# Kernel tuning notes

Measured on AMD Instinct MI355X. Metric: run time of the kernel, lower is better.

Reference implementation:

```python
import jax, jax.numpy as jnp
import numpy as np

N_NODES = 20000
N_EDGES = 400000
B = 4            # number of edge_attr tensors in the Python loop (batch of graphs)
NODE_DIM = 256   # == hidden_dim (required: forward feeds raw x into edge_fc)
EDGE_DIM = 16
HIDDEN = 256
OUT_DIM = 128


def setup_inputs() -> dict:
    key = jax.random.key(0)
    ks = jax.random.split(key, 6)
    x = jax.random.normal(ks[0], (N_NODES, NODE_DIM), dtype=jnp.float32)
    edge_index = jax.random.randint(ks[1], (2, N_EDGES), 0, N_NODES, dtype=jnp.int64)
    edge_attrs = jax.random.normal(ks[2], (B, N_EDGES, EDGE_DIM), dtype=jnp.float32)
    fan_in = 2 * HIDDEN + EDGE_DIM  # edge_fc in_features
    W_edge = jax.random.normal(ks[3], (fan_in, HIDDEN), dtype=jnp.float32) / np.sqrt(fan_in).astype(np.float32)
    b_edge = jnp.zeros((HIDDEN,), dtype=jnp.float32)
    W_graph = jax.random.normal(ks[4], (HIDDEN, OUT_DIM), dtype=jnp.float32) / np.sqrt(HIDDEN).astype(np.float32)
    b_graph = jnp.zeros((OUT_DIM,), dtype=jnp.float32)
    return {"x": x, "edge_index": edge_index, "edge_attrs": edge_attrs,
            "W_edge": W_edge, "b_edge": b_edge, "W_graph": W_graph, "b_graph": b_graph}


def reference(x, edge_index, edge_attrs, W_edge, b_edge, W_graph, b_graph):
    # Original: for each edge_attr in edge_attrs:
    #   relu(cat([x[src], x[dst], edge_attr]) @ W_edge + b).mean(0) @ W_graph + b_graph
    # Equivalent: split W_edge by the concat blocks; the (src,dst) contribution is
    # shared across the batch, so compute it once and broadcast.
    D = x.shape[1]
    W_src, W_dst, W_attr = W_edge[:D], W_edge[D:2 * D], W_edge[2 * D:]
    src = x[edge_index[0]]                      # [E, D] gather
    dst = x[edge_index[1]]                      # [E, D] gather
    base = src @ W_src + dst @ W_dst + b_edge   # [E, H]
    h = jax.nn.relu(base[None, :, :] + jnp.einsum('bea,ah->beh', edge_attrs, W_attr))  # [B, E, H]
    graph_feat = h.mean(axis=1)                 # [B, H] mean pool over edges
    return graph_feat @ W_graph + b_graph       # [B, OUT]
```

## Files before the change

kernel.cpp:

```cpp
#include <hip/hip_runtime.h>

#define N_NODES 20000
#define N_EDGES 400000
#define NODE_DIM 256
#define HIDDEN 256
#define OUT_DIM 128
#define PROJ_BLOCKS 628
#define CONV_BLOCKS 1024
#define EDGE_GRID 3125
#define NPART 8
#define ROWP 40

typedef __attribute__((ext_vector_type(8))) short short8;
typedef __attribute__((ext_vector_type(4))) float f32x4;

__device__ inline unsigned short f2bf(float f) {
  union { float f; unsigned u; } v; v.f = f;
  unsigned r = (v.u + 0x7FFFu + ((v.u >> 16) & 1u)) >> 16;
  return (unsigned short)r;
}

__global__ __launch_bounds__(256) void proj_mfma(
    const float* __restrict__ x, const float* __restrict__ We,
    const float* __restrict__ be, unsigned short* __restrict__ C,
    float* __restrict__ partial, const float* __restrict__ attrs,
    unsigned short* __restrict__ attrs_bf) {
  const int tid = threadIdx.x;
  if (blockIdx.x >= PROJ_BLOCKS) {
    const int nt = CONV_BLOCKS * 256;
    const int total4 = 4 * N_EDGES * 16 / 4;
    for (int i = (blockIdx.x - PROJ_BLOCKS) * 256 + tid; i < total4; i += nt) {
      float4 v = ((const float4*)attrs)[i];
      ushort4 o;
      o.x = f2bf(v.x); o.y = f2bf(v.y); o.z = f2bf(v.z); o.w = f2bf(v.w);
      ((ushort4*)attrs_bf)[i] = o;
    }
    return;
  }
  if (blockIdx.x == 0) {
    for (int i = tid; i < NPART * 4 * HIDDEN; i += 256) partial[i] = 0.f;
  }
  const int bm = blockIdx.x >> 2;
  const int bn = blockIdx.x & 3;
  const int row0 = bm * 128;
  const int col0 = bn * 128;
  const int half = col0 >> 8;
  const int ncol0 = col0 & 255;
  const int lane = tid & 63, wave = tid >> 6;
  const int q = lane >> 4, c = lane & 15;
  const int wm = wave >> 1, wn = wave & 1;

  __shared__ unsigned short As[128 * ROWP];
  __shared__ unsigned short Bs[128 * ROWP];

  f32x4 acc[4][4];
#pragma unroll
  for (int i = 0; i < 4; ++i)
#pragma unroll
    for (int t = 0; t < 4; ++t) acc[i][t] = (f32x4){0.f, 0.f, 0.f, 0.f};

  const int ar = tid >> 1;
  const int ak = (tid & 1) * 16;

  for (int k0 = 0; k0 < NODE_DIM; k0 += 32) {
    {
      const int r = row0 + ar;
      short8 t0, t1;
      if (r < N_NODES) {
        const float4* src = (const float4*)&x[(size_t)r * NODE_DIM + k0 + ak];
        float4 f0 = src[0], f1 = src[1], f2 = src[2], f3 = src[3];
        t0[0]=f2bf(f0.x); t0[1]=f2bf(f0.y); t0[2]=f2bf(f0.z); t0[3]=f2bf(f0.w);
        t0[4]=f2bf(f1.x); t0[5]=f2bf(f1.y); t0[6]=f2bf(f1.z); t0[7]=f2bf(f1.w);
        t1[0]=f2bf(f2.x); t1[1]=f2bf(f2.y); t1[2]=f2bf(f2.z); t1[3]=f2bf(f2.w);
        t1[4]=f2bf(f3.x); t1[5]=f2bf(f3.y); t1[6]=f2bf(f3.z); t1[7]=f2bf(f3.w);
      } else {
#pragma unroll
        for (int j = 0; j < 8; ++j) { t0[j] = 0; t1[j] = 0; }
      }
      *(short8*)&As[ar * ROWP + ak] = t0;
      *(short8*)&As[ar * ROWP + ak + 8] = t1;
    }
    {
#pragma unroll
      for (int s = 0; s < 2; ++s) {
        const int tau = tid + 256 * s;
        const int kp = ((tau >> 6) & 3) * 8;
        const int n  = (tau & 63) + ((tau >> 8) << 6);
        short8 bb;
#pragma unroll
        for (int j = 0; j < 8; ++j)
          bb[j] = (short)f2bf(
              We[(size_t)(half * 256 + k0 + kp + j) * HIDDEN + ncol0 + n]);
        *(short8*)&Bs[n * ROWP + kp] = bb;
      }
    }
    __syncthreads();
    short8 Af[4], Bf[4];
#pragma unroll
    for (int i = 0; i < 4; ++i)
      Af[i] = *(const short8*)&As[(wm * 64 + i * 16 + c) * ROWP + q * 8];
#pragma unroll
    for (int t = 0; t < 4; ++t)
      Bf[t] = *(const short8*)&Bs[(wn * 64 + t * 16 + c) * ROWP + q * 8];
#pragma unroll
    for (int i = 0; i < 4; ++i)
#pragma unroll
      for (int t = 0; t < 4; ++t)
        acc[i][t] = __builtin_amdgcn_mfma_f32_16x16x32_bf16(Af[i], Bf[t], acc[i][t], 0, 0, 0);
    __syncthreads();
  }

  float biasv[4] = {0.f, 0.f, 0.f, 0.f};
  const int nbase = ncol0 + wn * 64;
  if (half) {
#pragma unroll
    for (int t = 0; t < 4; ++t) biasv[t] = be[nbase + t * 16 + c];
  }
#pragma unroll
  for (int i = 0; i < 4; ++i) {
#pragma unroll
    for (int r = 0; r < 4; ++r) {
      const int node = row0 + wm * 64 + i * 16 + q * 4 + r;
      if (node < N_NODES) {
        ushort4 o;
        o.x = f2bf(acc[i][0][r] + biasv[0]);
        o.y = f2bf(acc[i][1][r] + biasv[1]);
        o.z = f2bf(acc[i][2][r] + biasv[2]);
        o.w = f2bf(acc[i][3][r] + biasv[3]);
        *(ushort4*)&C[(size_t)node * 512 + half * 256 + nbase + c * 4] = o;
      }
    }
  }
}

template <bool PRE>
__global__ __launch_bounds__(256) void edge_mfma(
    const unsigned short* __restrict__ C, const int* __restrict__ ei,
    const float* __restrict__ attrs_f, const unsigned short* __restrict__ attrs_b,
    const float* __restrict__ We, float* __restrict__ partial) {
  const int tid = threadIdx.x;
  const int lane = tid & 63, wave = tid >> 6;
  const int q = lane >> 4, c = lane & 15;
  const int hb = wave * 64;

  short8 Bf[4];
#pragma unroll
  for (int t = 0; t < 4; ++t) {
    short8 bf;
#pragma unroll
    for (int j = 0; j < 8; ++j) {
      int k = q * 8 + j;
      float w = (k < 16) ? We[(size_t)(512 + k) * HIDDEN + hb + t * 16 + c] : 0.0f;
      bf[j] = (short)f2bf(w);
    }
    Bf[t] = bf;
  }

  f32x4 accs[4];
#pragma unroll
  for (int b = 0; b < 4; ++b) accs[b] = (f32x4){0.f, 0.f, 0.f, 0.f};

  const f32x4 zero4 = {0.f, 0.f, 0.f, 0.f};
  const int ngroups = N_EDGES / 16;
  for (int g = blockIdx.x; g < ngroups; g += gridDim.x) {
    const int e0 = g * 16;
    const int4 ns4 = *(const int4*)&ei[e0 + q * 4];
    const int4 nd4 = *(const int4*)&ei[N_EDGES + e0 + q * 4];

    short8 Af[4];
    if (PRE) {
      if (q < 2) {
#pragma unroll
        for (int b = 0; b < 4; ++b)
          Af[b] = *(const short8*)&attrs_b[((size_t)b * N_EDGES + e0 + c) * 16 + q * 8];
      } else {
        short8 z;
#pragma unroll
        for (int j = 0; j < 8; ++j) z[j] = 0;
#pragma unroll
        for (int b = 0; b < 4; ++b) Af[b] = z;
      }
    } else {
      if (q < 2) {
#pragma unroll
        for (int b = 0; b < 4; ++b) {
          const size_t off = ((size_t)b * N_EDGES + e0 + c) * 16 + q * 8;
          const float4 a0 = *(const float4*)&attrs_f[off];
          const float4 a1 = *(const float4*)&attrs_f[off + 4];
          short8 af;
          af[0]=f2bf(a0.x); af[1]=f2bf(a0.y); af[2]=f2bf(a0.z); af[3]=f2bf(a0.w);
          af[4]=f2bf(a1.x); af[5]=f2bf(a1.y); af[6]=f2bf(a1.z); af[7]=f2bf(a1.w);
          Af[b] = af;
        }
      } else {
        short8 z;
#pragma unroll
        for (int j = 0; j < 8; ++j) z[j] = 0;
#pragma unroll
        for (int b = 0; b < 4; ++b) Af[b] = z;
      }
    }

    f32x4 base4[4];
    {
      const int nn[4] = {ns4.x, ns4.y, ns4.z, ns4.w};
      const int dd[4] = {nd4.x, nd4.y, nd4.z, nd4.w};
#pragma unroll
      for (int r = 0; r < 4; ++r) {
        const uint2 s = *(const uint2*)&C[(size_t)nn[r] * 512 + hb + c * 4];
        const uint2 d = *(const uint2*)&C[(size_t)dd[r] * 512 + 256 + hb + c * 4];
        base4[0][r] = __uint_as_float(s.x << 16) + __uint_as_float(d.x << 16);
        base4[1][r] = __uint_as_float(s.x & 0xFFFF0000u) + __uint_as_float(d.x & 0xFFFF0000u);
        base4[2][r] = __uint_as_float(s.y << 16) + __uint_as_float(d.y << 16);
        base4[3][r] = __uint_as_float(s.y & 0xFFFF0000u) + __uint_as_float(d.y & 0xFFFF0000u);
      }
    }

#pragma unroll
    for (int b = 0; b < 4; ++b) {
#pragma unroll
      for (int t = 0; t < 4; ++t) {
        f32x4 S = __builtin_amdgcn_mfma_f32_16x16x32_bf16(Af[b], Bf[t], zero4, 0, 0, 0);
        f32x4 u = S + base4[t];
        u[0] = fmaxf(u[0], 0.f); u[1] = fmaxf(u[1], 0.f);
        u[2] = fmaxf(u[2], 0.f); u[3] = fmaxf(u[3], 0.f);
        accs[b][t] += (u[0] + u[1]) + (u[2] + u[3]);
      }
    }
  }

  float* pp = partial + (size_t)(blockIdx.x & (NPART - 1)) * (4 * HIDDEN);
#pragma unroll
  for (int b = 0; b < 4; ++b)
#pragma unroll
    for (int t = 0; t < 4; ++t) {
      float v = accs[b][t];
      v += __shfl_xor(v, 16, 64);
      v += __shfl_xor(v, 32, 64);
      if (q == 0) atomicAdd(&pp[b * HIDDEN + hb + t * 16 + c], v);
    }
}

__global__ __launch_bounds__(256) void graph_out(
    const float* __restrict__ partial, const float* __restrict__ Wg,
    const float* __restrict__ bg, float* __restrict__ out) {
  const int o = blockIdx.x;
  const int hh = threadIdx.x;
  const int lane = hh & 63, wave = hh >> 6;
  const float w = Wg[(size_t)hh * OUT_DIM + o];
  float v[4];
#pragma unroll
  for (int b = 0; b < 4; ++b) {
    float s = 0.f;
#pragma unroll
    for (int k = 0; k < NPART; ++k) s += partial[k * 4 * HIDDEN + b * HIDDEN + hh];
    v[b] = s * w;
  }
#pragma unroll
  for (int off = 32; off >= 1; off >>= 1)
#pragma unroll
    for (int b = 0; b < 4; ++b) v[b] += __shfl_down(v[b], off, 64);
  __shared__ float red[4][4];
  if (lane == 0)
#pragma unroll
    for (int b = 0; b < 4; ++b) red[wave][b] = v[b];
  __syncthreads();
  if (hh < 4) {
    float s = red[0][hh] + red[1][hh] + red[2][hh] + red[3][hh];
    out[hh * OUT_DIM + o] = s * (1.0f / (float)N_EDGES) + bg[o];
  }
}

extern "C" void kernel_launch(void* const* d_in, const int* in_sizes, int n_in,
                              void* d_out, int out_size, void* d_ws, size_t ws_size,
                              hipStream_t stream) {
  const float* x  = (const float*)d_in[0];
  const int*   ei = (const int*)d_in[1];
  const float* ea = (const float*)d_in[2];
  const float* We = (const float*)d_in[3];
  const float* be = (const float*)d_in[4];
  const float* Wg = (const float*)d_in[5];
  const float* bg = (const float*)d_in[6];
  float* out = (float*)d_out;

  const size_t C_bytes = (size_t)N_NODES * 512 * 2;
  const size_t A_bytes = (size_t)4 * N_EDGES * 16 * 2;
  const size_t P_bytes = (size_t)NPART * 4 * HIDDEN * 4;
  unsigned short* C = (unsigned short*)d_ws;
  const bool pre = ws_size >= C_bytes + A_bytes + P_bytes + 4096;
  unsigned short* attrs_bf = pre ? (unsigned short*)((char*)d_ws + C_bytes) : nullptr;
  float* partial = (float*)((char*)d_ws + (pre ? C_bytes + A_bytes : C_bytes));

  const int grid1 = pre ? PROJ_BLOCKS + CONV_BLOCKS : PROJ_BLOCKS;
  proj_mfma<<<grid1, 256, 0, stream>>>(x, We, be, C, partial, ea, attrs_bf);
  if (pre)
    edge_mfma<true><<<EDGE_GRID, 256, 0, stream>>>(C, ei, nullptr, attrs_bf, We, partial);
  else
    edge_mfma<false><<<EDGE_GRID, 256, 0, stream>>>(C, ei, ea, nullptr, We, partial);
  graph_out<<<128, 256, 0, stream>>>(partial, Wg, bg, out);
}
```

Baseline: 268.6 us.

## Use K=16 bf16 MFMA and prefetch next edge indices in edge kernel

Switches the attribute MFMA from the 16x16x32 variant, which had half its K dimension zero-padded, to the 16x16x16 bf16 variant so every lane loads four real attribute values and there are no zero-fill branches. Edge indices for the next group are now loaded one iteration ahead, and the gathers of C rows are issued before the attribute loads, to hide index-load latency behind the dependent gathers. This adds register pressure from the prefetched indices and gathered values, and the smaller MFMA may have different throughput.

```diff
diff --git a/kernel.cpp b/kernel.cpp
--- a/kernel.cpp
+++ b/kernel.cpp
@@ -12,6 +12,7 @@
 #define ROWP 40
 
 typedef __attribute__((ext_vector_type(8))) short short8;
+typedef __attribute__((ext_vector_type(4))) short bf16x4;
 typedef __attribute__((ext_vector_type(4))) float f32x4;
 
 __device__ inline unsigned short f2bf(float f) {
@@ -141,18 +142,16 @@
   const int tid = threadIdx.x;
   const int lane = tid & 63, wave = tid >> 6;
   const int q = lane >> 4, c = lane & 15;
+  const int q4 = q * 4;
   const int hb = wave * 64;
 
-  short8 Bf[4];
+  bf16x4 Bf[4];
 #pragma unroll
   for (int t = 0; t < 4; ++t) {
-    short8 bf;
-#pragma unroll
-    for (int j = 0; j < 8; ++j) {
-      int k = q * 8 + j;
-      float w = (k < 16) ? We[(size_t)(512 + k) * HIDDEN + hb + t * 16 + c] : 0.0f;
-      bf[j] = (short)f2bf(w);
-    }
+    bf16x4 bf;
+#pragma unroll
+    for (int j = 0; j < 4; ++j)
+      bf[j] = (short)f2bf(We[(size_t)(512 + q4 + j) * HIDDEN + hb + t * 16 + c]);
     Bf[t] = bf;
   }
 
@@ -162,65 +161,60 @@
 
   const f32x4 zero4 = {0.f, 0.f, 0.f, 0.f};
   const int ngroups = N_EDGES / 16;
+
+  int4 ns4 = *(const int4*)&ei[blockIdx.x * 16 + q * 4];
+  int4 nd4 = *(const int4*)&ei[N_EDGES + blockIdx.x * 16 + q * 4];
+
   for (int g = blockIdx.x; g < ngroups; g += gridDim.x) {
     const int e0 = g * 16;
-    const int4 ns4 = *(const int4*)&ei[e0 + q * 4];
-    const int4 nd4 = *(const int4*)&ei[N_EDGES + e0 + q * 4];
-
-    short8 Af[4];
-    if (PRE) {
-      if (q < 2) {
-#pragma unroll
-        for (int b = 0; b < 4; ++b)
-          Af[b] = *(const short8*)&attrs_b[((size_t)b * N_EDGES + e0 + c) * 16 + q * 8];
-      } else {
-        short8 z;
-#pragma unroll
-        for (int j = 0; j < 8; ++j) z[j] = 0;
-#pragma unroll
-        for (int b = 0; b < 4; ++b) Af[b] = z;
-      }
-    } else {
-      if (q < 2) {
-#pragma unroll
-        for (int b = 0; b < 4; ++b) {
-          const size_t off = ((size_t)b * N_EDGES + e0 + c) * 16 + q * 8;
-          const float4 a0 = *(const float4*)&attrs_f[off];
-          const float4 a1 = *(const float4*)&attrs_f[off + 4];
-          short8 af;
-          af[0]=f2bf(a0.x); af[1]=f2bf(a0.y); af[2]=f2bf(a0.z); af[3]=f2bf(a0.w);
-          af[4]=f2bf(a1.x); af[5]=f2bf(a1.y); af[6]=f2bf(a1.z); af[7]=f2bf(a1.w);
-          Af[b] = af;
-        }
-      } else {
-        short8 z;
-#pragma unroll
-        for (int j = 0; j < 8; ++j) z[j] = 0;
-#pragma unroll
-        for (int b = 0; b < 4; ++b) Af[b] = z;
-      }
-    }
-
-    f32x4 base4[4];
+    const int gn = g + gridDim.x;
+
+    uint2 sv[4], dv[4];
     {
       const int nn[4] = {ns4.x, ns4.y, ns4.z, ns4.w};
       const int dd[4] = {nd4.x, nd4.y, nd4.z, nd4.w};
 #pragma unroll
       for (int r = 0; r < 4; ++r) {
-        const uint2 s = *(const uint2*)&C[(size_t)nn[r] * 512 + hb + c * 4];
-        const uint2 d = *(const uint2*)&C[(size_t)dd[r] * 512 + 256 + hb + c * 4];
-        base4[0][r] = __uint_as_float(s.x << 16) + __uint_as_float(d.x << 16);
-        base4[1][r] = __uint_as_float(s.x & 0xFFFF0000u) + __uint_as_float(d.x & 0xFFFF0000u);
-        base4[2][r] = __uint_as_float(s.y << 16) + __uint_as_float(d.y << 16);
-        base4[3][r] = __uint_as_float(s.y & 0xFFFF0000u) + __uint_as_float(d.y & 0xFFFF0000u);
-      }
+        sv[r] = *(const uint2*)&C[(size_t)nn[r] * 512 + hb + c * 4];
+        dv[r] = *(const uint2*)&C[(size_t)dd[r] * 512 + 256 + hb + c * 4];
+      }
+    }
+    if (gn < ngroups) {
+      ns4 = *(const int4*)&ei[gn * 16 + q * 4];
+      nd4 = *(const int4*)&ei[N_EDGES + gn * 16 + q * 4];
+    }
+
+    bf16x4 Af[4];
+    if (PRE) {
+#pragma unroll
+      for (int b = 0; b < 4; ++b)
+        Af[b] = *(const bf16x4*)&attrs_b[((size_t)b * N_EDGES + e0 + c) * 16 + q4];
+    } else {
+#pragma unroll
+      for (int b = 0; b < 4; ++b) {
+        const size_t off = ((size_t)b * N_EDGES + e0 + c) * 16 + q4;
+        const float4 a0 = *(const float4*)&attrs_f[off];
+        bf16x4 af;
+        af[0]=f2bf(a0.x); af[1]=f2bf(a0.y); af[2]=f2bf(a0.z); af[3]=f2bf(a0.w);
+        Af[b] = af;
+      }
+    }
+
+    f32x4 base4[4];
+#pragma unroll
+    for (int r = 0; r < 4; ++r) {
+      const uint2 s = sv[r], d = dv[r];
+      base4[0][r] = __uint_as_float(s.x << 16) + __uint_as_float(d.x << 16);
+      base4[1][r] = __uint_as_float(s.x & 0xFFFF0000u) + __uint_as_float(d.x & 0xFFFF0000u);
+      base4[2][r] = __uint_as_float(s.y << 16) + __uint_as_float(d.y << 16);
+      base4[3][r] = __uint_as_float(s.y & 0xFFFF0000u) + __uint_as_float(d.y & 0xFFFF0000u);
     }
 
 #pragma unroll
     for (int b = 0; b < 4; ++b) {
 #pragma unroll
       for (int t = 0; t < 4; ++t) {
-        f32x4 S = __builtin_amdgcn_mfma_f32_16x16x32_bf16(Af[b], Bf[t], zero4, 0, 0, 0);
+        f32x4 S = __builtin_amdgcn_mfma_f32_16x16x16bf16_1k(Af[b], Bf[t], zero4, 0, 0, 0);
         f32x4 u = S + base4[t];
         u[0] = fmaxf(u[0], 0.f); u[1] = fmaxf(u[1], 0.f);
         u[2] = fmaxf(u[2], 0.f); u[3] = fmaxf(u[3], 0.f);
```

Measured after the change: 262.3 us. -2.3%, faster.
